# Kernel tuning notes

Measured on AMD Instinct MI355X. Metric: run time of the kernel, lower is better.

## Reference

```python
import jax, jax.numpy as jnp
import numpy as np

D_MODEL = 64
N_HEADS = 4
D_HEAD = D_MODEL // N_HEADS
LN_EPS = 1e-5


def setup_inputs() -> dict:
    key = jax.random.key(0)
    ks = jax.random.split(key, 10)
    d = D_MODEL
    s = 1.0 / np.sqrt(d)
    X = jax.random.normal(ks[0], (4, 256, 200, d), dtype=jnp.float32)
    Wq = jax.random.uniform(ks[1], (d, d), jnp.float32, -s, s)
    bq = jax.random.uniform(ks[2], (d,), jnp.float32, -s, s)
    Wk = jax.random.uniform(ks[3], (d, d), jnp.float32, -s, s)
    bk = jax.random.uniform(ks[4], (d,), jnp.float32, -s, s)
    Wv = jax.random.uniform(ks[5], (d, d), jnp.float32, -s, s)
    bv = jax.random.uniform(ks[6], (d,), jnp.float32, -s, s)
    Wo = jax.random.uniform(ks[7], (d, d), jnp.float32, -s, s)
    bo = jax.random.uniform(ks[8], (d,), jnp.float32, -s, s)
    gamma = jnp.ones((d,), jnp.float32)
    beta = jnp.zeros((d,), jnp.float32)
    return {"X": X, "Wq": Wq, "bq": bq, "Wk": Wk, "bk": bk,
            "Wv": Wv, "bv": bv, "Wo": Wo, "bo": bo,
            "gamma": gamma, "beta": beta}


def reference(X, Wq, bq, Wk, bk, Wv, bv, Wo, bo, gamma, beta):
    B, T, N, d = X.shape
    H, dh = N_HEADS, D_HEAD
    # [B, T, N, d] -> [B*N, T, d]
    Xbn = jnp.transpose(X, (0, 2, 1, 3)).reshape(B * N, T, d)
    Q = Xbn @ Wq + bq
    K = Xbn @ Wk + bk
    V = Xbn @ Wv + bv

    def split(x):  # [BN, T, d] -> [BN, H, T, dh]
        return jnp.transpose(x.reshape(B * N, T, H, dh), (0, 2, 1, 3))

    Qh, Kh, Vh = split(Q), split(K), split(V)
    scores = jnp.einsum('bhtd,bhsd->bhts', Qh, Kh) / np.sqrt(dh).astype(np.float32)
    attn = jax.nn.softmax(scores, axis=-1)  # dropout is identity at eval
    out_h = jnp.einsum('bhts,bhsd->bhtd', attn, Vh)
    out = jnp.transpose(out_h, (0, 2, 1, 3)).reshape(B * N, T, d)
    out = out @ Wo + bo
    out = out + Xbn
    # LayerNorm over last dim
    mu = jnp.mean(out, axis=-1, keepdims=True)
    var = jnp.var(out, axis=-1, keepdims=True)
    out = (out - mu) * jax.lax.rsqrt(var + LN_EPS) * gamma + beta
    # [B*N, T, d] -> [B, T, N, d]
    return jnp.transpose(out.reshape(B, N, T, d), (0, 2, 1, 3))
```

## Files before the change

### kernel.cpp

```cpp
#include <hip/hip_runtime.h>
#include <hip/hip_bf16.h>
#include <hip/hip_fp8.h>

constexpr int B_ = 4, T_ = 256, N_ = 200, D_ = 64, H_ = 4;
constexpr int BN_ = B_ * N_;
constexpr float LN_EPS = 1e-5f;
constexpr float QSCALE = 0.25f * 1.4426950408889634f;

typedef short short8_t __attribute__((ext_vector_type(8)));
typedef float f32x4 __attribute__((ext_vector_type(4)));

#if __has_builtin(__builtin_amdgcn_exp2f)
#define EXP2(x) __builtin_amdgcn_exp2f(x)
#else
#define EXP2(x) exp2f(x)
#endif

constexpr int OFF_Q  = 0;
constexpr int OFF_K  = 24576;
constexpr int OFF_V  = 49152;
constexpr int OFF_WT = 66560;
constexpr int ARENA_BYTES = 75776;

__device__ __forceinline__ ushort f2bf(float f) {
    union { float f; unsigned u; } v; v.f = f;
    unsigned u = v.u + 0x7FFFu + ((v.u >> 16) & 1u);
    return (ushort)(u >> 16);
}

template <bool HI>
__device__ __forceinline__ unsigned cvt2fp8(float a, float b, unsigned old) {
#if __has_builtin(__builtin_amdgcn_cvt_pk_fp8_f32)
    return __builtin_amdgcn_cvt_pk_fp8_f32(a, b, old, HI);
#else
    __hip_fp8_e4m3 fa(a), fb(b);
    unsigned v = (unsigned)fa.__x | ((unsigned)fb.__x << 8);
    return HI ? ((old & 0x0000FFFFu) | (v << 16)) : ((old & 0xFFFF0000u) | v);
#endif
}

__device__ __forceinline__ f32x4 mfma_fp8(long long a, long long b, f32x4 c) {
    return __builtin_amdgcn_mfma_f32_16x16x32_fp8_fp8(a, b, c, 0, 0, 0);
}

__global__ __launch_bounds__(512, 4) void fused_attn_kernel(
    const float* __restrict__ X,
    const float* __restrict__ Wq, const float* __restrict__ bq,
    const float* __restrict__ Wk, const float* __restrict__ bk,
    const float* __restrict__ Wv, const float* __restrict__ bv,
    const float* __restrict__ Wo, const float* __restrict__ bo,
    const float* __restrict__ gamma, const float* __restrict__ beta,
    float* __restrict__ out)
{
    __shared__ __align__(16) unsigned char arena[ARENA_BYTES];
    unsigned char* Qf8 = arena + OFF_Q;
    unsigned char* Kf8 = arena + OFF_K;
    unsigned char* Vf8 = arena + OFF_V;
    ushort* sWT   = (ushort*)(arena + OFF_WT);
    ushort* sAttn = (ushort*)arena;

    const int bn   = blockIdx.x;
    const int b    = bn / N_;
    const int n    = bn - b * N_;
    const int tid  = threadIdx.x;
    const int lane = tid & 63;
    const int w    = tid >> 6;
    const int lm   = lane & 15;
    const int g    = lane >> 4;
    const int wbase = w * 32;

    const f32x4 zz = {0.f, 0.f, 0.f, 0.f};

    short8_t af[2][2];
    #pragma unroll
    for (int mt = 0; mt < 2; ++mt) {
        #pragma unroll
        for (int kf = 0; kf < 2; ++kf) {
            const int t = wbase + mt * 16 + lm;
            const float* xp = X + (((long)(b * T_ + t)) * N_ + n) * D_ + kf * 32 + 8 * g;
            const float4 x0 = *(const float4*)xp;
            const float4 x1 = *(const float4*)(xp + 4);
            union { short8_t v; unsigned u[4]; } tmp;
            tmp.u[0] = ((unsigned)f2bf(x0.y) << 16) | f2bf(x0.x);
            tmp.u[1] = ((unsigned)f2bf(x0.w) << 16) | f2bf(x0.z);
            tmp.u[2] = ((unsigned)f2bf(x1.y) << 16) | f2bf(x1.x);
            tmp.u[3] = ((unsigned)f2bf(x1.w) << 16) | f2bf(x1.z);
            af[mt][kf] = tmp.v;
        }
    }

    const float* Wm[3] = {Wq, Wk, Wv};
    const float* bm[3] = {bq, bk, bv};
    #pragma unroll 1
    for (int m = 0; m < 3; ++m) {
        for (int idx = tid; idx < 4096; idx += 512) {
            const int k = idx >> 6, c = idx & 63;
            sWT[c * 72 + k] = f2bf(Wm[m][idx]);
        }
        __syncthreads();

        short8_t bf[4][2];
        #pragma unroll
        for (int nt = 0; nt < 4; ++nt)
            #pragma unroll
            for (int kf = 0; kf < 2; ++kf)
                bf[nt][kf] = *(const short8_t*)&sWT[(nt * 16 + lm) * 72 + kf * 32 + 8 * g];

        if (m < 2) {
            f32x4 accT[4][2];
            #pragma unroll
            for (int dt = 0; dt < 4; ++dt)
                #pragma unroll
                for (int q2 = 0; q2 < 2; ++q2) {
                    accT[dt][q2] = zz;
                    #pragma unroll
                    for (int kf = 0; kf < 2; ++kf)
                        accT[dt][q2] = __builtin_amdgcn_mfma_f32_16x16x32_bf16(
                            bf[dt][kf], af[q2][kf], accT[dt][q2], 0, 0, 0);
                }
            __syncthreads();

            unsigned char* dst = (m == 0) ? Qf8 : Kf8;
            const float scl = (m == 0) ? QSCALE : 1.0f;
            #pragma unroll
            for (int dt = 0; dt < 4; ++dt) {
                const float4 bI = *(const float4*)(bm[m] + dt * 16 + 4 * g);
                #pragma unroll
                for (int q2 = 0; q2 < 2; ++q2) {
                    const float v0 = (accT[dt][q2][0] + bI.x) * scl;
                    const float v1 = (accT[dt][q2][1] + bI.y) * scl;
                    const float v2 = (accT[dt][q2][2] + bI.z) * scl;
                    const float v3 = (accT[dt][q2][3] + bI.w) * scl;
                    unsigned pk = cvt2fp8<false>(v0, v1, 0u);
                    pk = cvt2fp8<true>(v2, v3, pk);
                    const int q = wbase + q2 * 16 + lm;
                    *(unsigned*)(dst + dt * 6144 + q * 24 + 4 * g) = pk;
                }
            }
        } else {
            f32x4 accV[2][4];
            #pragma unroll
            for (int mt = 0; mt < 2; ++mt)
                #pragma unroll
                for (int nt = 0; nt < 4; ++nt) {
                    accV[mt][nt] = zz;
                    #pragma unroll
                    for (int kf = 0; kf < 2; ++kf)
                        accV[mt][nt] = __builtin_amdgcn_mfma_f32_16x16x32_bf16(
                            af[mt][kf], bf[nt][kf], accV[mt][nt], 0, 0, 0);
                }
            __syncthreads();

            #pragma unroll
            for (int nt = 0; nt < 4; ++nt) {
                const float blv = bm[2][nt * 16 + lm];
                #pragma unroll
                for (int mt = 0; mt < 2; ++mt) {
                    const float v0 = accV[mt][nt][0] + blv;
                    const float v1 = accV[mt][nt][1] + blv;
                    const float v2 = accV[mt][nt][2] + blv;
                    const float v3 = accV[mt][nt][3] + blv;
                    unsigned pk = cvt2fp8<false>(v0, v1, 0u);
                    pk = cvt2fp8<true>(v2, v3, pk);
                    *(unsigned*)(Vf8 + (nt * 16 + lm) * 272 + wbase + mt * 16 + 4 * g) = pk;
                }
            }
        }
    }

    for (int idx = tid; idx < 4096; idx += 512) {
        const int k = idx >> 6, c = idx & 63;
        sWT[c * 72 + k] = f2bf(Wo[idx]);
    }
    __syncthreads();

    const int h     = w >> 1;
    const int qbase = (w & 1) * 128;
    const bool glo  = (g < 2);

    long long qf[8];
    #pragma unroll
    for (int qt = 0; qt < 8; ++qt)
        qf[qt] = glo ? *(const long long*)(Qf8 + h * 6144 + (qbase + qt * 16 + lm) * 24 + 8 * g)
                     : 0ll;

    f32x4 oacc[8];
    float lsum[8];
    #pragma unroll
    for (int qt = 0; qt < 8; ++qt) { oacc[qt] = zz; lsum[qt] = 0.f; }

    #pragma unroll 1
    for (int c = 0; c < 8; ++c) {
        const long long kfe = glo ? *(const long long*)(Kf8 + h * 6144 + ((2 * c) * 16 + lm) * 24 + 8 * g) : 0ll;
        const long long kfo = glo ? *(const long long*)(Kf8 + h * 6144 + ((2 * c + 1) * 16 + lm) * 24 + 8 * g) : 0ll;
        const unsigned va = *(const unsigned*)(Vf8 + (h * 16 + lm) * 272 + 32 * c + 4 * g);
        const unsigned vb = *(const unsigned*)(Vf8 + (h * 16 + lm) * 272 + 32 * c + 16 + 4 * g);
        const long long vf = (long long)(((unsigned long long)vb << 32) | va);

        #pragma unroll
        for (int qt = 0; qt < 8; ++qt) {
            const f32x4 se = mfma_fp8(kfe, qf[qt], zz);
            const f32x4 so = mfma_fp8(kfo, qf[qt], zz);
            const float pe0 = EXP2(se[0]), pe1 = EXP2(se[1]);
            const float pe2 = EXP2(se[2]), pe3 = EXP2(se[3]);
            const float po0 = EXP2(so[0]), po1 = EXP2(so[1]);
            const float po2 = EXP2(so[2]), po3 = EXP2(so[3]);
            lsum[qt] += ((pe0 + pe1) + (pe2 + pe3)) + ((po0 + po1) + (po2 + po3));
            unsigned a0 = cvt2fp8<false>(pe0, pe1, 0u); a0 = cvt2fp8<true>(pe2, pe3, a0);
            unsigned a1 = cvt2fp8<false>(po0, po1, 0u); a1 = cvt2fp8<true>(po2, po3, a1);
            const long long pa = (long long)(((unsigned long long)a1 << 32) | a0);
            oacc[qt] = mfma_fp8(pa, vf, oacc[qt]);
        }
    }

    float inv[8];
    #pragma unroll
    for (int qt = 0; qt < 8; ++qt) {
        float t0 = lsum[qt] + __shfl_xor(lsum[qt], 16, 64);
        t0 += __shfl_xor(t0, 32, 64);
        inv[qt] = 1.0f / t0;
    }

    __syncthreads();

    #pragma unroll
    for (int qt = 0; qt < 8; ++qt)
        #pragma unroll
        for (int r = 0; r < 4; ++r) {
            const float iv = __shfl(inv[qt], 4 * g + r, 64);
            sAttn[(qbase + qt * 16 + 4 * g + r) * 72 + h * 16 + lm] = f2bf(oacc[qt][r] * iv);
        }

    __syncthreads();

    short8_t wf[4][2];
    #pragma unroll
    for (int nt = 0; nt < 4; ++nt)
        #pragma unroll
        for (int kf = 0; kf < 2; ++kf)
            wf[nt][kf] = *(const short8_t*)&sWT[(nt * 16 + lm) * 72 + kf * 32 + 8 * g];

    short8_t aF[2][2];
    #pragma unroll
    for (int mt = 0; mt < 2; ++mt)
        #pragma unroll
        for (int kf = 0; kf < 2; ++kf)
            aF[mt][kf] = *(const short8_t*)&sAttn[(wbase + mt * 16 + lm) * 72 + kf * 32 + 8 * g];

    f32x4 acc2[2][4];
    #pragma unroll
    for (int mt = 0; mt < 2; ++mt)
        #pragma unroll
        for (int nt = 0; nt < 4; ++nt) {
            acc2[mt][nt] = zz;
            #pragma unroll
            for (int kf = 0; kf < 2; ++kf)
                acc2[mt][nt] = __builtin_amdgcn_mfma_f32_16x16x32_bf16(
                    aF[mt][kf], wf[nt][kf], acc2[mt][nt], 0, 0, 0);
        }

    float bo_l[4], ga_l[4], be_l[4];
    #pragma unroll
    for (int nt = 0; nt < 4; ++nt) {
        bo_l[nt] = bo[nt * 16 + lm];
        ga_l[nt] = gamma[nt * 16 + lm];
        be_l[nt] = beta[nt * 16 + lm];
    }

    #pragma unroll
    for (int mt = 0; mt < 2; ++mt)
        #pragma unroll
        for (int r = 0; r < 4; ++r) {
            const int t = wbase + mt * 16 + 4 * g + r;
            const long base = (((long)(b * T_ + t)) * N_ + n) * D_;
            float v[4];
            #pragma unroll
            for (int nt = 0; nt < 4; ++nt)
                v[nt] = acc2[mt][nt][r] + bo_l[nt] + X[base + nt * 16 + lm];
            float s1 = (v[0] + v[1]) + (v[2] + v[3]);
            float s2 = (v[0] * v[0] + v[1] * v[1]) + (v[2] * v[2] + v[3] * v[3]);
            #pragma unroll
            for (int m = 1; m <= 8; m <<= 1) {
                s1 += __shfl_xor(s1, m, 64);
                s2 += __shfl_xor(s2, m, 64);
            }
            const float mu  = s1 * 0.015625f;
            const float var = s2 * 0.015625f - mu * mu;
            const float rs  = rsqrtf(var + LN_EPS);
            #pragma unroll
            for (int nt = 0; nt < 4; ++nt)
                out[base + nt * 16 + lm] = (v[nt] - mu) * rs * ga_l[nt] + be_l[nt];
        }
}

extern "C" void kernel_launch(void* const* d_in, const int* in_sizes, int n_in,
                              void* d_out, int out_size, void* d_ws, size_t ws_size,
                              hipStream_t stream) {
    const float* X     = (const float*)d_in[0];
    const float* Wq    = (const float*)d_in[1];
    const float* bq    = (const float*)d_in[2];
    const float* Wk    = (const float*)d_in[3];
    const float* bk    = (const float*)d_in[4];
    const float* Wv    = (const float*)d_in[5];
    const float* bv    = (const float*)d_in[6];
    const float* Wo    = (const float*)d_in[7];
    const float* bo    = (const float*)d_in[8];
    const float* gamma = (const float*)d_in[9];
    const float* beta  = (const float*)d_in[10];

    fused_attn_kernel<<<BN_, 512, 0, stream>>>(
        X, Wq, bq, Wk, bk, Wv, bv, Wo, bo, gamma, beta, (float*)d_out);
}
```

Baseline: 71.12 us.

## Shrink LDS arena by aliasing weight staging and repacking Q/K rows

Cuts the shared-memory arena by dropping the padding on fp8 Q/K rows (stride 24 to 16) and aliasing the weight-transpose staging buffer onto the Q region. The projection order becomes K, V, Q so Q is written last, and Wo staging moves into the attention epilogue. The launch-bounds occupancy hint rises to allow more resident blocks per CU. Weight transposes now write packed pairs of bf16 as 32-bit stores. The unpadded Q/K stride risks more LDS bank conflicts, and tighter register limits could cause spills.

```diff
diff --git a/kernel.cpp b/kernel.cpp
--- a/kernel.cpp
+++ b/kernel.cpp
@@ -16,11 +16,10 @@
 #define EXP2(x) exp2f(x)
 #endif
 
-constexpr int OFF_Q  = 0;
-constexpr int OFF_K  = 24576;
-constexpr int OFF_V  = 49152;
-constexpr int OFF_WT = 66560;
-constexpr int ARENA_BYTES = 75776;
+constexpr int OFF_K  = 16384;
+constexpr int OFF_V  = 32768;
+constexpr int OFF_WO = 36864;
+constexpr int ARENA_BYTES = 50176;
 
 __device__ __forceinline__ ushort f2bf(float f) {
     union { float f; unsigned u; } v; v.f = f;
@@ -43,7 +42,7 @@
     return __builtin_amdgcn_mfma_f32_16x16x32_fp8_fp8(a, b, c, 0, 0, 0);
 }
 
-__global__ __launch_bounds__(512, 4) void fused_attn_kernel(
+__global__ __launch_bounds__(512, 6) void fused_attn_kernel(
     const float* __restrict__ X,
     const float* __restrict__ Wq, const float* __restrict__ bq,
     const float* __restrict__ Wk, const float* __restrict__ bk,
@@ -53,11 +52,12 @@
     float* __restrict__ out)
 {
     __shared__ __align__(16) unsigned char arena[ARENA_BYTES];
-    unsigned char* Qf8 = arena + OFF_Q;
+    unsigned char* Qf8 = arena;
     unsigned char* Kf8 = arena + OFF_K;
     unsigned char* Vf8 = arena + OFF_V;
-    ushort* sWT   = (ushort*)(arena + OFF_WT);
+    ushort* sWT   = (ushort*)arena;
     ushort* sAttn = (ushort*)arena;
+    ushort* sWoT  = (ushort*)(arena + OFF_WO);
 
     const int bn   = blockIdx.x;
     const int b    = bn / N_;
@@ -89,13 +89,15 @@
         }
     }
 
-    const float* Wm[3] = {Wq, Wk, Wv};
-    const float* bm[3] = {bq, bk, bv};
+    const float* Wm[3] = {Wk, Wv, Wq};
+    const float* bm[3] = {bk, bv, bq};
     #pragma unroll 1
     for (int m = 0; m < 3; ++m) {
-        for (int idx = tid; idx < 4096; idx += 512) {
-            const int k = idx >> 6, c = idx & 63;
-            sWT[c * 72 + k] = f2bf(Wm[m][idx]);
+        for (int idx = tid; idx < 2048; idx += 512) {
+            const int c = idx & 63, kp = idx >> 6;
+            const unsigned lo = f2bf(Wm[m][(2 * kp) * 64 + c]);
+            const unsigned hi = f2bf(Wm[m][(2 * kp + 1) * 64 + c]);
+            *(unsigned*)&sWT[c * 72 + 2 * kp] = lo | (hi << 16);
         }
         __syncthreads();
 
@@ -106,7 +108,9 @@
             for (int kf = 0; kf < 2; ++kf)
                 bf[nt][kf] = *(const short8_t*)&sWT[(nt * 16 + lm) * 72 + kf * 32 + 8 * g];
 
-        if (m < 2) {
+        __syncthreads();
+
+        if (m != 1) {
             f32x4 accT[4][2];
             #pragma unroll
             for (int dt = 0; dt < 4; ++dt)
@@ -118,10 +122,9 @@
                         accT[dt][q2] = __builtin_amdgcn_mfma_f32_16x16x32_bf16(
                             bf[dt][kf], af[q2][kf], accT[dt][q2], 0, 0, 0);
                 }
-            __syncthreads();
-
-            unsigned char* dst = (m == 0) ? Qf8 : Kf8;
-            const float scl = (m == 0) ? QSCALE : 1.0f;
+
+            unsigned char* dst = (m == 0) ? Kf8 : Qf8;
+            const float scl = (m == 2) ? QSCALE : 1.0f;
             #pragma unroll
             for (int dt = 0; dt < 4; ++dt) {
                 const float4 bI = *(const float4*)(bm[m] + dt * 16 + 4 * g);
@@ -134,7 +137,7 @@
                     unsigned pk = cvt2fp8<false>(v0, v1, 0u);
                     pk = cvt2fp8<true>(v2, v3, pk);
                     const int q = wbase + q2 * 16 + lm;
-                    *(unsigned*)(dst + dt * 6144 + q * 24 + 4 * g) = pk;
+                    *(unsigned*)(dst + dt * 4096 + q * 16 + 4 * g) = pk;
                 }
             }
         } else {
@@ -149,11 +152,10 @@
                         accV[mt][nt] = __builtin_amdgcn_mfma_f32_16x16x32_bf16(
                             af[mt][kf], bf[nt][kf], accV[mt][nt], 0, 0, 0);
                 }
-            __syncthreads();
 
             #pragma unroll
             for (int nt = 0; nt < 4; ++nt) {
-                const float blv = bm[2][nt * 16 + lm];
+                const float blv = bm[1][nt * 16 + lm];
                 #pragma unroll
                 for (int mt = 0; mt < 2; ++mt) {
                     const float v0 = accV[mt][nt][0] + blv;
@@ -168,10 +170,6 @@
         }
     }
 
-    for (int idx = tid; idx < 4096; idx += 512) {
-        const int k = idx >> 6, c = idx & 63;
-        sWT[c * 72 + k] = f2bf(Wo[idx]);
-    }
     __syncthreads();
 
     const int h     = w >> 1;
@@ -181,7 +179,7 @@
     long long qf[8];
     #pragma unroll
     for (int qt = 0; qt < 8; ++qt)
-        qf[qt] = glo ? *(const long long*)(Qf8 + h * 6144 + (qbase + qt * 16 + lm) * 24 + 8 * g)
+        qf[qt] = glo ? *(const long long*)(Qf8 + h * 4096 + (qbase + qt * 16 + lm) * 16 + 8 * g)
                      : 0ll;
 
     f32x4 oacc[8];
@@ -191,8 +189,8 @@
 
     #pragma unroll 1
     for (int c = 0; c < 8; ++c) {
-        const long long kfe = glo ? *(const long long*)(Kf8 + h * 6144 + ((2 * c) * 16 + lm) * 24 + 8 * g) : 0ll;
-        const long long kfo = glo ? *(const long long*)(Kf8 + h * 6144 + ((2 * c + 1) * 16 + lm) * 24 + 8 * g) : 0ll;
+        const long long kfe = glo ? *(const long long*)(Kf8 + h * 4096 + ((2 * c) * 16 + lm) * 16 + 8 * g) : 0ll;
+        const long long kfo = glo ? *(const long long*)(Kf8 + h * 4096 + ((2 * c + 1) * 16 + lm) * 16 + 8 * g) : 0ll;
         const unsigned va = *(const unsigned*)(Vf8 + (h * 16 + lm) * 272 + 32 * c + 4 * g);
         const unsigned vb = *(const unsigned*)(Vf8 + (h * 16 + lm) * 272 + 32 * c + 16 + 4 * g);
         const long long vf = (long long)(((unsigned long long)vb << 32) | va);
@@ -230,6 +228,12 @@
             const float iv = __shfl(inv[qt], 4 * g + r, 64);
             sAttn[(qbase + qt * 16 + 4 * g + r) * 72 + h * 16 + lm] = f2bf(oacc[qt][r] * iv);
         }
+    for (int idx = tid; idx < 2048; idx += 512) {
+        const int c = idx & 63, kp = idx >> 6;
+        const unsigned lo = f2bf(Wo[(2 * kp) * 64 + c]);
+        const unsigned hi = f2bf(Wo[(2 * kp + 1) * 64 + c]);
+        *(unsigned*)&sWoT[c * 72 + 2 * kp] = lo | (hi << 16);
+    }
 
     __syncthreads();
 
@@ -238,7 +242,7 @@
     for (int nt = 0; nt < 4; ++nt)
         #pragma unroll
         for (int kf = 0; kf < 2; ++kf)
-            wf[nt][kf] = *(const short8_t*)&sWT[(nt * 16 + lm) * 72 + kf * 32 + 8 * g];
+            wf[nt][kf] = *(const short8_t*)&sWoT[(nt * 16 + lm) * 72 + kf * 32 + 8 * g];
 
     short8_t aF[2][2];
     #pragma unroll
```

Result: slower. 104.5 us (+46.9%).

## Split attention into two query passes and compute softmax sums via MFMA

Applied to the files above, without the earlier changes.

The attention loop now handles 64 queries per pass over two passes instead of 128 at once, which shrinks the live register set. Row sums of the softmax numerators are computed by an extra FP8 MFMA against a ones vector instead of scalar adds and cross-lane shuffles. It also uses a hardware reciprocal, raises wave priority around the MFMA/exp block, and moves one barrier ahead of the projection MFMAs. In exchange, K/V fragments are reloaded from LDS in each pass, MFMA count rises, and the sums are taken over FP8-rounded probabilities, which slightly changes numerics.

```diff
diff --git a/kernel.cpp b/kernel.cpp
--- a/kernel.cpp
+++ b/kernel.cpp
@@ -14,6 +14,12 @@
 #define EXP2(x) __builtin_amdgcn_exp2f(x)
 #else
 #define EXP2(x) exp2f(x)
+#endif
+
+#if __has_builtin(__builtin_amdgcn_rcpf)
+#define RCP(x) __builtin_amdgcn_rcpf(x)
+#else
+#define RCP(x) (1.0f / (x))
 #endif
 
 constexpr int OFF_Q  = 0;
@@ -106,6 +112,8 @@
             for (int kf = 0; kf < 2; ++kf)
                 bf[nt][kf] = *(const short8_t*)&sWT[(nt * 16 + lm) * 72 + kf * 32 + 8 * g];
 
+        __syncthreads();
+
         if (m < 2) {
             f32x4 accT[4][2];
             #pragma unroll
@@ -118,7 +126,6 @@
                         accT[dt][q2] = __builtin_amdgcn_mfma_f32_16x16x32_bf16(
                             bf[dt][kf], af[q2][kf], accT[dt][q2], 0, 0, 0);
                 }
-            __syncthreads();
 
             unsigned char* dst = (m == 0) ? Qf8 : Kf8;
             const float scl = (m == 0) ? QSCALE : 1.0f;
@@ -149,7 +156,6 @@
                         accV[mt][nt] = __builtin_amdgcn_mfma_f32_16x16x32_bf16(
                             af[mt][kf], bf[nt][kf], accV[mt][nt], 0, 0, 0);
                 }
-            __syncthreads();
 
             #pragma unroll
             for (int nt = 0; nt < 4; ++nt) {
@@ -178,58 +184,75 @@
     const int qbase = (w & 1) * 128;
     const bool glo  = (g < 2);
 
-    long long qf[8];
-    #pragma unroll
-    for (int qt = 0; qt < 8; ++qt)
-        qf[qt] = glo ? *(const long long*)(Qf8 + h * 6144 + (qbase + qt * 16 + lm) * 24 + 8 * g)
-                     : 0ll;
-
-    f32x4 oacc[8];
-    float lsum[8];
-    #pragma unroll
-    for (int qt = 0; qt < 8; ++qt) { oacc[qt] = zz; lsum[qt] = 0.f; }
+    const long long ONES8 = 0x3838383838383838ll;
+
+    f32x4 oacc[4], lacc[4];
+    unsigned pend[8];
 
     #pragma unroll 1
-    for (int c = 0; c < 8; ++c) {
-        const long long kfe = glo ? *(const long long*)(Kf8 + h * 6144 + ((2 * c) * 16 + lm) * 24 + 8 * g) : 0ll;
-        const long long kfo = glo ? *(const long long*)(Kf8 + h * 6144 + ((2 * c + 1) * 16 + lm) * 24 + 8 * g) : 0ll;
-        const unsigned va = *(const unsigned*)(Vf8 + (h * 16 + lm) * 272 + 32 * c + 4 * g);
-        const unsigned vb = *(const unsigned*)(Vf8 + (h * 16 + lm) * 272 + 32 * c + 16 + 4 * g);
-        const long long vf = (long long)(((unsigned long long)vb << 32) | va);
-
-        #pragma unroll
-        for (int qt = 0; qt < 8; ++qt) {
-            const f32x4 se = mfma_fp8(kfe, qf[qt], zz);
-            const f32x4 so = mfma_fp8(kfo, qf[qt], zz);
-            const float pe0 = EXP2(se[0]), pe1 = EXP2(se[1]);
-            const float pe2 = EXP2(se[2]), pe3 = EXP2(se[3]);
-            const float po0 = EXP2(so[0]), po1 = EXP2(so[1]);
-            const float po2 = EXP2(so[2]), po3 = EXP2(so[3]);
-            lsum[qt] += ((pe0 + pe1) + (pe2 + pe3)) + ((po0 + po1) + (po2 + po3));
-            unsigned a0 = cvt2fp8<false>(pe0, pe1, 0u); a0 = cvt2fp8<true>(pe2, pe3, a0);
-            unsigned a1 = cvt2fp8<false>(po0, po1, 0u); a1 = cvt2fp8<true>(po2, po3, a1);
-            const long long pa = (long long)(((unsigned long long)a1 << 32) | a0);
-            oacc[qt] = mfma_fp8(pa, vf, oacc[qt]);
-        }
-    }
-
-    float inv[8];
-    #pragma unroll
-    for (int qt = 0; qt < 8; ++qt) {
-        float t0 = lsum[qt] + __shfl_xor(lsum[qt], 16, 64);
-        t0 += __shfl_xor(t0, 32, 64);
-        inv[qt] = 1.0f / t0;
+    for (int pass = 0; pass < 2; ++pass) {
+        const int qoff = qbase + pass * 64;
+        long long qf[4];
+        #pragma unroll
+        for (int qt = 0; qt < 4; ++qt)
+            qf[qt] = glo ? *(const long long*)(Qf8 + h * 6144 + (qoff + qt * 16 + lm) * 24 + 8 * g)
+                         : 0ll;
+        #pragma unroll
+        for (int qt = 0; qt < 4; ++qt) { oacc[qt] = zz; lacc[qt] = zz; }
+
+        #pragma unroll 1
+        for (int c = 0; c < 8; ++c) {
+            const long long kfe = glo ? *(const long long*)(Kf8 + h * 6144 + ((2 * c) * 16 + lm) * 24 + 8 * g) : 0ll;
+            const long long kfo = glo ? *(const long long*)(Kf8 + h * 6144 + ((2 * c + 1) * 16 + lm) * 24 + 8 * g) : 0ll;
+            const unsigned va = *(const unsigned*)(Vf8 + (h * 16 + lm) * 272 + 32 * c + 4 * g);
+            const unsigned vb = *(const unsigned*)(Vf8 + (h * 16 + lm) * 272 + 32 * c + 16 + 4 * g);
+            const long long vf = (long long)(((unsigned long long)vb << 32) | va);
+
+            __builtin_amdgcn_s_setprio(1);
+            #pragma unroll
+            for (int qt = 0; qt < 4; ++qt) {
+                const f32x4 se = mfma_fp8(kfe, qf[qt], zz);
+                const f32x4 so = mfma_fp8(kfo, qf[qt], zz);
+                const float pe0 = EXP2(se[0]), pe1 = EXP2(se[1]);
+                const float pe2 = EXP2(se[2]), pe3 = EXP2(se[3]);
+                const float po0 = EXP2(so[0]), po1 = EXP2(so[1]);
+                const float po2 = EXP2(so[2]), po3 = EXP2(so[3]);
+                unsigned a0 = cvt2fp8<false>(pe0, pe1, 0u); a0 = cvt2fp8<true>(pe2, pe3, a0);
+                unsigned a1 = cvt2fp8<false>(po0, po1, 0u); a1 = cvt2fp8<true>(po2, po3, a1);
+                const long long pa = (long long)(((unsigned long long)a1 << 32) | a0);
+                oacc[qt] = mfma_fp8(pa, vf, oacc[qt]);
+                lacc[qt] = mfma_fp8(pa, ONES8, lacc[qt]);
+            }
+            __builtin_amdgcn_s_setprio(0);
+        }
+
+        if (pass == 0) {
+            #pragma unroll
+            for (int qt = 0; qt < 4; ++qt) {
+                pend[2 * qt] = ((unsigned)f2bf(oacc[qt][1] * RCP(lacc[qt][1])) << 16) |
+                               f2bf(oacc[qt][0] * RCP(lacc[qt][0]));
+                pend[2 * qt + 1] = ((unsigned)f2bf(oacc[qt][3] * RCP(lacc[qt][3])) << 16) |
+                                   f2bf(oacc[qt][2] * RCP(lacc[qt][2]));
+            }
+        }
     }
 
     __syncthreads();
 
     #pragma unroll
-    for (int qt = 0; qt < 8; ++qt)
-        #pragma unroll
-        for (int r = 0; r < 4; ++r) {
-            const float iv = __shfl(inv[qt], 4 * g + r, 64);
-            sAttn[(qbase + qt * 16 + 4 * g + r) * 72 + h * 16 + lm] = f2bf(oacc[qt][r] * iv);
-        }
+    for (int qt = 0; qt < 4; ++qt) {
+        const int row0 = qbase + qt * 16 + 4 * g;
+        sAttn[(row0 + 0) * 72 + h * 16 + lm] = (ushort)(pend[2 * qt] & 0xFFFFu);
+        sAttn[(row0 + 1) * 72 + h * 16 + lm] = (ushort)(pend[2 * qt] >> 16);
+        sAttn[(row0 + 2) * 72 + h * 16 + lm] = (ushort)(pend[2 * qt + 1] & 0xFFFFu);
+        sAttn[(row0 + 3) * 72 + h * 16 + lm] = (ushort)(pend[2 * qt + 1] >> 16);
+    }
+    #pragma unroll
+    for (int qt = 0; qt < 4; ++qt)
+        #pragma unroll
+        for (int r = 0; r < 4; ++r)
+            sAttn[(qbase + 64 + qt * 16 + 4 * g + r) * 72 + h * 16 + lm] =
+                f2bf(oacc[qt][r] * RCP(lacc[qt][r]));
 
     __syncthreads();
 
```

New measurement: 72.19 us. Within noise of the previous version (+1.5%).
